# Kernel tuning notes

Hardware: AMD Instinct MI355X
Metric: run time of the kernel (lower is better)

The kernel has to match this reference:

```python
import jax, jax.numpy as jnp
import numpy as np

EPS = 1e-6
NUM_HEADS = 16
ROPE_THETA = 100000.0


def _rope_tables(seq_len, head_dim, theta):
    inv_freq = 1.0 / (theta ** (np.arange(0, head_dim, 2, dtype=np.float32) / head_dim))
    t = np.arange(seq_len, dtype=np.float32)
    freqs = np.outer(t, inv_freq)                      # (S, head_dim//2)
    emb = np.concatenate([freqs, freqs], axis=-1)      # (S, head_dim)
    return jnp.asarray(np.cos(emb))[None], jnp.asarray(np.sin(emb))[None]  # (1,S,D)


def setup_inputs() -> dict:
    key = jax.random.key(0)
    ks = jax.random.split(key, 6)
    B, S, H = 2, 2048, 1024
    head_dim = H // NUM_HEADS
    cos, sin = _rope_tables(S, head_dim, ROPE_THETA)
    scale = 0.02
    return {
        "hidden_states": jax.random.normal(ks[0], (B, S, H), dtype=jnp.float32),
        "cos": cos, "sin": sin,
        "Wq": jax.random.normal(ks[1], (H, H), dtype=jnp.float32) * scale,
        "bq": jnp.zeros((H,), dtype=jnp.float32),
        "Wk": jax.random.normal(ks[2], (H, H), dtype=jnp.float32) * scale,
        "bk": jnp.zeros((H,), dtype=jnp.float32),
        "Wv": jax.random.normal(ks[3], (H, H), dtype=jnp.float32) * scale,
        "bv": jnp.zeros((H,), dtype=jnp.float32),
        "Wo": jax.random.normal(ks[4], (H, H), dtype=jnp.float32) * scale,
        "bo": jnp.zeros((H,), dtype=jnp.float32),
        "rms_weight": jnp.ones((H,), dtype=jnp.float32),
    }


def _rms_norm(x, w):
    var = jnp.mean(x * x, axis=-1, keepdims=True)
    return x * jax.lax.rsqrt(var + EPS) * w


def _rotate_half(x):
    x1, x2 = jnp.split(x, 2, axis=-1)
    return jnp.concatenate([-x2, x1], axis=-1)


def reference(hidden_states, cos, sin, Wq, bq, Wk, bk, Wv, bv, Wo, bo, rms_weight):
    B, S, H = hidden_states.shape
    D = H // NUM_HEADS
    q = hidden_states @ Wq.T + bq
    k = hidden_states @ Wk.T + bk
    v = hidden_states @ Wv.T + bv
    # RMSNorm over full hidden dim BEFORE head split (as in original)
    q = _rms_norm(q, rms_weight)
    k = _rms_norm(k, rms_weight)
    # (B,S,H) -> (B,heads,S,D)
    q = q.reshape(B, S, NUM_HEADS, D).transpose(0, 2, 1, 3)
    k = k.reshape(B, S, NUM_HEADS, D).transpose(0, 2, 1, 3)
    v = v.reshape(B, S, NUM_HEADS, D).transpose(0, 2, 1, 3)
    # RoPE: cos/sin (1,S,D) -> unsqueeze head dim
    c = cos[:, None, :, :]
    s = sin[:, None, :, :]
    q = q * c + _rotate_half(q) * s
    k = k * c + _rotate_half(k) * s
    # attention (faithful: boolean tril mask is ADDED as 0/1, not -inf)
    scale = D ** 0.5
    scores = jnp.einsum("bhqd,bhkd->bhqk", q, k) / scale
    mask = jnp.tril(jnp.ones((S, S), dtype=scores.dtype))  # +1 on causal, +0 elsewhere
    attn = jax.nn.softmax(scores + mask, axis=-1)
    out = jnp.einsum("bhqk,bhkd->bhqd", attn, v)
    out = out.transpose(0, 2, 1, 3).reshape(B, S, H)
    return out @ Wo.T + bo
```

## Files before the change

kernel.cpp:

```cpp
#include <hip/hip_runtime.h>

typedef unsigned short u16;
typedef __attribute__((ext_vector_type(8))) _Float16 half8;
typedef __attribute__((ext_vector_type(2))) __fp16 fp16x2;
typedef __attribute__((ext_vector_type(4))) float f32x4;
typedef __attribute__((ext_vector_type(16))) float f32x16;

#define MFMAH(A,B,C) __builtin_amdgcn_mfma_f32_16x16x32_f16(A,B,C,0,0,0)
#define MFMA32(A,B,C) __builtin_amdgcn_mfma_f32_32x32x16_f16(A,B,C,0,0,0)
#define LOG2E 1.4426950408889634f
#define C1 0.18033688011112042f

__device__ __forceinline__ u16 f2h(float f){
  _Float16 h = (_Float16)f; u16 r; __builtin_memcpy(&r,&h,2); return r;
}
__device__ __forceinline__ float h2f(u16 v){
  _Float16 h; __builtin_memcpy(&h,&v,2); return (float)h;
}
__device__ __forceinline__ unsigned int pack_h2(float a, float b){
  fp16x2 h = __builtin_amdgcn_cvt_pkrtz(a,b);
  unsigned int r; __builtin_memcpy(&r,&h,4); return r;
}

__device__ __forceinline__ void async_ld16(const void* g, void* l) {
  __builtin_amdgcn_global_load_lds(
      (const __attribute__((address_space(1))) unsigned int*)g,
      (__attribute__((address_space(3))) unsigned int*)l, 16, 0, 0);
}

__global__ __launch_bounds__(256) void cast_all(const float* __restrict__ hs,
    const float* __restrict__ wq, const float* __restrict__ wk,
    const float* __restrict__ wv, const float* __restrict__ wo,
    u16* __restrict__ dst)
{
  unsigned int i = blockIdx.x*256 + threadIdx.x;
  size_t el = (size_t)i * 8;
  const float* src; size_t off;
  if (el < 4194304) { src = hs; off = el; }
  else {
    unsigned int r = (unsigned int)((el - 4194304) >> 20);
    src = (r==0)?wq:(r==1)?wk:(r==2)?wv:wo;
    off = (el - 4194304) & 1048575;
  }
  float4 a = *reinterpret_cast<const float4*>(src+off);
  float4 b = *reinterpret_cast<const float4*>(src+off+4);
  uint4 o = {pack_h2(a.x,a.y), pack_h2(a.z,a.w), pack_h2(b.x,b.y), pack_h2(b.z,b.w)};
  *reinterpret_cast<uint4*>(dst + el) = o;
}

__global__ __launch_bounds__(256) void gemm_qkv(const u16* __restrict__ A,
                                                const u16* __restrict__ W,
                                                const float* __restrict__ bqp,
                                                const float* __restrict__ bkp,
                                                const float* __restrict__ bvp,
                                                u16* __restrict__ qout,
                                                u16* __restrict__ kout,
                                                u16* __restrict__ vout,
                                                int M, int K)
{
  __shared__ __align__(16) u16 lds_a[128*32];
  __shared__ __align__(16) u16 lds_w[128*32];
  const int t = threadIdx.x;
  const int lane = t & 63, wave = t >> 6;
  const int wm = wave >> 1, wn = wave & 1;
  const int lr = lane & 15, quad = lane >> 4;
  const int flat = blockIdx.x;
  const int xcd = flat & 7, slot = flat >> 3;
  const int ln = slot % 12, lm = slot / 12;
  const int n0 = ((xcd & 1) * 12 + ln) * 128;
  const int m0 = ((xcd >> 1) * 8 + lm) * 128;
  const int wbase = t & 192;
  const int which = n0 >> 10;

  const f32x4 fzero = {0.f,0.f,0.f,0.f};
  f32x4 acc[4][4];
  #pragma unroll
  for (int i=0;i<4;++i)
    #pragma unroll
    for (int j=0;j<4;++j) acc[i][j] = fzero;

  if (which < 2) {
    for (int k0 = 0; k0 < K; k0 += 32) {
      __syncthreads();
      #pragma unroll
      for (int it=0; it<2; ++it) {
        int idx = it*256 + t;
        int row = idx >> 2, c8 = (idx & 3) * 8;
        int lbase = (it*256 + wbase) * 8;
        async_ld16(&A[(size_t)(m0+row)*K + k0 + c8], &lds_a[lbase]);
        async_ld16(&W[(size_t)(n0+row)*K + k0 + c8], &lds_w[lbase]);
      }
      __syncthreads();
      half8 af[4], bfr[4];
      #pragma unroll
      for (int mt=0; mt<4; ++mt)
        af[mt] = *reinterpret_cast<const half8*>(&lds_a[(wm*64 + mt*16 + lr)*32 + quad*8]);
      #pragma unroll
      for (int nt=0; nt<4; ++nt)
        bfr[nt] = *reinterpret_cast<const half8*>(&lds_w[(wn*64 + nt*16 + lr)*32 + quad*8]);
      #pragma unroll
      for (int mt=0; mt<4; ++mt)
        #pragma unroll
        for (int nt=0; nt<4; ++nt)
          acc[mt][nt] = MFMAH(bfr[nt], af[mt], acc[mt][nt]);
    }
    const float* bp = which ? bkp : bqp;
    u16* dst = which ? kout : qout;
    #pragma unroll
    for (int nt=0; nt<4; ++nt) {
      int nn = (n0 & 1023) + wn*64 + nt*16 + quad*4;
      float4 bv = *reinterpret_cast<const float4*>(&bp[nn]);
      int hh = nn >> 6, d4 = nn & 63;
      #pragma unroll
      for (int mt=0; mt<4; ++mt) {
        int m = m0 + wm*64 + mt*16 + lr;
        int b = m >> 11, s = m & 2047;
        uint2 o = {pack_h2(acc[mt][nt][0]+bv.x, acc[mt][nt][1]+bv.y),
                   pack_h2(acc[mt][nt][2]+bv.z, acc[mt][nt][3]+bv.w)};
        *reinterpret_cast<uint2*>(&dst[((size_t)(b*16 + hh)*2048 + s)*64 + d4]) = o;
      }
    }
  } else {
    for (int k0 = 0; k0 < K; k0 += 32) {
      __syncthreads();
      #pragma unroll
      for (int it=0; it<2; ++it) {
        int idx = it*256 + t;
        int row = idx >> 2, c8 = (idx & 3) * 8;
        int lbase = (it*256 + wbase) * 8;
        async_ld16(&A[(size_t)(m0+row)*K + k0 + c8], &lds_a[lbase]);
        async_ld16(&W[(size_t)(n0+row)*K + k0 + c8], &lds_w[lbase]);
      }
      __syncthreads();
      half8 af[4], bfr[4];
      #pragma unroll
      for (int mt=0; mt<4; ++mt)
        af[mt] = *reinterpret_cast<const half8*>(&lds_a[(wm*64 + mt*16 + lr)*32 + quad*8]);
      #pragma unroll
      for (int nt=0; nt<4; ++nt)
        bfr[nt] = *reinterpret_cast<const half8*>(&lds_w[(wn*64 + nt*16 + lr)*32 + quad*8]);
      #pragma unroll
      for (int mt=0; mt<4; ++mt)
        #pragma unroll
        for (int nt=0; nt<4; ++nt)
          acc[mt][nt] = MFMAH(af[mt], bfr[nt], acc[mt][nt]);
    }
    #pragma unroll
    for (int nt=0; nt<4; ++nt) {
      int nn = (n0 & 1023) + wn*64 + nt*16 + lr;
      float bv = bvp[nn];
      int hh = nn >> 6, d = nn & 63;
      #pragma unroll
      for (int mt=0; mt<4; ++mt) {
        int m = m0 + wm*64 + mt*16 + quad*4;
        int b = m >> 11, s = m & 2047;
        uint2 o = {pack_h2(acc[mt][nt][0]+bv, acc[mt][nt][1]+bv),
                   pack_h2(acc[mt][nt][2]+bv, acc[mt][nt][3]+bv)};
        *reinterpret_cast<uint2*>(&vout[((size_t)(b*16 + hh)*64 + d)*2048 + s]) = o;
      }
    }
  }
}

__global__ __launch_bounds__(256) void gemm_o(const u16* __restrict__ A,
                                              const u16* __restrict__ W,
                                              const float* __restrict__ bias,
                                              float* __restrict__ O,
                                              int M, int N, int K)
{
  __shared__ __align__(16) u16 lds_a[128*32];
  __shared__ __align__(16) u16 lds_w[64*32];
  const int t = threadIdx.x;
  const int lane = t & 63, wm = t >> 6;
  const int lr = lane & 15, quad = lane >> 4;
  const int flat = blockIdx.x;
  const int xcd = flat & 7, slot = flat >> 3;
  const int n0 = (slot & 15) * 64;
  const int m0 = ((xcd << 2) + (slot >> 4)) * 128;
  const int wbase = t & 192;

  const f32x4 fzero = {0.f,0.f,0.f,0.f};
  f32x4 acc[2][4];
  #pragma unroll
  for (int i=0;i<2;++i)
    #pragma unroll
    for (int j=0;j<4;++j) acc[i][j] = fzero;

  for (int k0 = 0; k0 < K; k0 += 32) {
    __syncthreads();
    #pragma unroll
    for (int it=0; it<2; ++it) {
      int idx = it*256 + t;
      int row = idx >> 2, c8 = (idx & 3) * 8;
      int lbase = (it*256 + wbase) * 8;
      async_ld16(&A[(size_t)(m0+row)*K + k0 + c8], &lds_a[lbase]);
    }
    async_ld16(&W[(size_t)(n0 + (t>>2))*K + k0 + (t&3)*8], &lds_w[wbase*8]);
    __syncthreads();
    half8 af[2], bfr[4];
    #pragma unroll
    for (int mt=0; mt<2; ++mt)
      af[mt] = *reinterpret_cast<const half8*>(&lds_a[(wm*32 + mt*16 + lr)*32 + quad*8]);
    #pragma unroll
    for (int nt=0; nt<4; ++nt)
      bfr[nt] = *reinterpret_cast<const half8*>(&lds_w[(nt*16 + lr)*32 + quad*8]);
    #pragma unroll
    for (int mt=0; mt<2; ++mt)
      #pragma unroll
      for (int nt=0; nt<4; ++nt)
        acc[mt][nt] = MFMAH(bfr[nt], af[mt], acc[mt][nt]);
  }

  #pragma unroll
  for (int nt=0; nt<4; ++nt) {
    int nb = n0 + nt*16 + quad*4;
    float4 bv = *reinterpret_cast<const float4*>(&bias[nb]);
    #pragma unroll
    for (int mt=0; mt<2; ++mt) {
      int m = m0 + wm*32 + mt*16 + lr;
      float4 o = {acc[mt][nt][0]+bv.x, acc[mt][nt][1]+bv.y,
                  acc[mt][nt][2]+bv.z, acc[mt][nt][3]+bv.w};
      *reinterpret_cast<float4*>(&O[(size_t)m * N + nb]) = o;
    }
  }
}

__global__ __launch_bounds__(256) void rmsrope(u16* __restrict__ qb, u16* __restrict__ kb,
                                               const float* __restrict__ cosb,
                                               const float* __restrict__ sinb,
                                               const float* __restrict__ w)
{
  const int bs = blockIdx.x;
  const int b = bs >> 11, s = bs & 2047;
  const int t = threadIdx.x;
  u16* buf = (t & 128) ? kb : qb;
  const int tl = t & 127;
  const int h = tl >> 3, d0 = (tl & 7) * 4;
  size_t base = ((size_t)(b*16+h)*2048 + s)*64;

  uint2 u1 = *reinterpret_cast<const uint2*>(&buf[base + d0]);
  uint2 u2 = *reinterpret_cast<const uint2*>(&buf[base + d0 + 32]);
  u16 a1[4], a2[4];
  __builtin_memcpy(a1, &u1, 8); __builtin_memcpy(a2, &u2, 8);
  float x1[4], x2[4];
  float ss = 0.f;
  #pragma unroll
  for (int j=0;j<4;++j){
    x1[j] = h2f(a1[j]); x2[j] = h2f(a2[j]);
    ss += x1[j]*x1[j] + x2[j]*x2[j];
  }
  #pragma unroll
  for (int off=32; off>0; off>>=1) ss += __shfl_xor(ss, off, 64);
  __shared__ float red[4];
  if ((t & 63) == 0) red[t>>6] = ss;
  __syncthreads();
  float tot = (t & 128) ? (red[2] + red[3]) : (red[0] + red[1]);
  float r = rsqrtf(tot * (1.0f/1024.0f) + 1e-6f);

  float4 w1 = *reinterpret_cast<const float4*>(&w[h*64+d0]);
  float4 w2 = *reinterpret_cast<const float4*>(&w[h*64+d0+32]);
  float4 c1 = *reinterpret_cast<const float4*>(&cosb[s*64+d0]);
  float4 s1 = *reinterpret_cast<const float4*>(&sinb[s*64+d0]);
  float4 c2 = *reinterpret_cast<const float4*>(&cosb[s*64+d0+32]);
  float4 s2 = *reinterpret_cast<const float4*>(&sinb[s*64+d0+32]);
  float n1[4] = {x1[0]*r*w1.x, x1[1]*r*w1.y, x1[2]*r*w1.z, x1[3]*r*w1.w};
  float n2[4] = {x2[0]*r*w2.x, x2[1]*r*w2.y, x2[2]*r*w2.z, x2[3]*r*w2.w};
  float o1[4] = {n1[0]*c1.x - n2[0]*s1.x, n1[1]*c1.y - n2[1]*s1.y,
                 n1[2]*c1.z - n2[2]*s1.z, n1[3]*c1.w - n2[3]*s1.w};
  float o2[4] = {n2[0]*c2.x + n1[0]*s2.x, n2[1]*c2.y + n1[1]*s2.y,
                 n2[2]*c2.z + n1[2]*s2.z, n2[3]*c2.w + n1[3]*s2.w};
  uint2 v1 = {pack_h2(o1[0],o1[1]), pack_h2(o1[2],o1[3])};
  uint2 v2 = {pack_h2(o2[0],o2[1]), pack_h2(o2[2],o2[3])};
  *reinterpret_cast<uint2*>(&buf[base + d0])      = v1;
  *reinterpret_cast<uint2*>(&buf[base + d0 + 32]) = v2;
}

__global__ __launch_bounds__(512, 2) void attn(const u16* __restrict__ qh,
                                               const u16* __restrict__ kh,
                                               const u16* __restrict__ vt,
                                               u16* __restrict__ ao)
{
  __shared__ __align__(16) u16 kbuf[2][2][64*72];
  __shared__ __align__(16) u16 vbuf[2][2][64*72];
  const int t = threadIdx.x;
  const int lane = t & 63, w = t >> 6;
  const int g = w >> 2, wq = w & 3;
  const int ql = lane & 31, hf = lane >> 5;
  const int flat = blockIdx.x;
  const int xcd = flat & 7, slot = flat >> 3;
  const int bh = xcd + ((slot >> 4) << 3);
  const int qbase = (slot & 15) * 128;
  const int b = bh >> 4, h = bh & 15;
  const size_t hb = (size_t)bh * 2048 * 64;
  const u16* qp = qh + hb;
  const u16* kp = kh + hb;
  const u16* vtp = vt + hb;

  const int q_abs = qbase + wq*32 + ql;
  half8 qf[4];
  #pragma unroll
  for (int s=0;s<4;++s)
    qf[s] = *reinterpret_cast<const half8*>(&qp[(size_t)q_abs*64 + s*16 + hf*8]);

  half8 onesf;
  #pragma unroll
  for (int i=0;i<8;++i) onesf[i] = (_Float16)1.0f;

  const int lt = t & 255;
  const int row = lt >> 3;
  const int cc = lt & 7;
  const int base2 = 32*(cc>>2) + 16*((cc>>1)&1) + 4*(cc&1);
  const int kofs = row*72 + cc*8;
  const u16* kg = kp + (size_t)(g*1024 + row)*64 + cc*8;
  const u16* vg = vtp + (size_t)row*2048 + g*1024 + base2;

  const f32x16 fz16 = {0.f,0.f,0.f,0.f,0.f,0.f,0.f,0.f,0.f,0.f,0.f,0.f,0.f,0.f,0.f,0.f};
  f32x16 oacc[2];
  oacc[0] = fz16; oacc[1] = fz16;
  f32x16 lacc = fz16;
  const int diag = (qbase + wq*32) >> 6;

  {
    uint4 k0v = *reinterpret_cast<const uint4*>(kg);
    uint4 k1v = *reinterpret_cast<const uint4*>(kg + 32*64);
    uint2 a0 = *reinterpret_cast<const uint2*>(vg);
    uint2 a1 = *reinterpret_cast<const uint2*>(vg + 8);
    uint2 b0 = *reinterpret_cast<const uint2*>(vg + (size_t)32*2048);
    uint2 b1 = *reinterpret_cast<const uint2*>(vg + (size_t)32*2048 + 8);
    *reinterpret_cast<uint4*>(&kbuf[g][0][kofs])        = k0v;
    *reinterpret_cast<uint4*>(&kbuf[g][0][kofs+32*72])  = k1v;
    uint4 v0 = {a0.x,a0.y,a1.x,a1.y};
    uint4 v1 = {b0.x,b0.y,b1.x,b1.y};
    *reinterpret_cast<uint4*>(&vbuf[g][0][kofs])        = v0;
    *reinterpret_cast<uint4*>(&vbuf[g][0][kofs+32*72])  = v1;
  }

  for (int kt=0; kt<16; ++kt) {
    __syncthreads();
    uint4 k0n, k1n; uint2 a0n, a1n, b0n, b1n;
    if (kt < 15) {
      const u16* kgn = kg + (size_t)(kt+1)*4096;
      const u16* vgn = vg + (kt+1)*64;
      k0n = *reinterpret_cast<const uint4*>(kgn);
      k1n = *reinterpret_cast<const uint4*>(kgn + 32*64);
      a0n = *reinterpret_cast<const uint2*>(vgn);
      a1n = *reinterpret_cast<const uint2*>(vgn + 8);
      b0n = *reinterpret_cast<const uint2*>(vgn + (size_t)32*2048);
      b1n = *reinterpret_cast<const uint2*>(vgn + (size_t)32*2048 + 8);
    }
    const u16* kb = &kbuf[g][kt & 1][0];
    const u16* vb = &vbuf[g][kt & 1][0];
    const int gkt = (g << 4) + kt;

    unsigned int pk[4][4];
    #pragma unroll
    for (int kh2=0; kh2<2; ++kh2) {
      f32x16 z = fz16;
      #pragma unroll
      for (int s=0;s<4;++s) {
        half8 kf;
        __builtin_memcpy(&kf, &kb[(kh2*32+ql)*72 + s*16 + hf*8], 16);
        z = MFMA32(kf, qf[s], z);
      }
      float p[16];
      if (gkt != diag) {
        float ml = (gkt < diag) ? LOG2E : 0.0f;
        #pragma unroll
        for (int r=0;r<16;++r)
          p[r] = __builtin_amdgcn_exp2f(__builtin_fmaf(z[r], C1, ml));
      } else {
        #pragma unroll
        for (int r=0;r<16;++r) {
          int key = gkt*64 + kh2*32 + (r&3) + 8*(r>>2) + 4*hf;
          float ml = (key <= q_abs) ? LOG2E : 0.0f;
          p[r] = __builtin_amdgcn_exp2f(__builtin_fmaf(z[r], C1, ml));
        }
      }
      #pragma unroll
      for (int t2=0;t2<2;++t2)
        #pragma unroll
        for (int jj=0;jj<4;++jj)
          pk[kh2*2+t2][jj] = pack_h2(p[t2*8+jj*2], p[t2*8+jj*2+1]);
    }

    #pragma unroll
    for (int st=0;st<4;++st) {
      uint4 pq = {pk[st][0], pk[st][1], pk[st][2], pk[st][3]};
      half8 pf; __builtin_memcpy(&pf, &pq, 16);
      lacc = MFMA32(onesf, pf, lacc);
      #pragma unroll
      for (int dh=0; dh<2; ++dh) {
        half8 vf;
        __builtin_memcpy(&vf, &vb[(dh*32+ql)*72 + st*16 + hf*8], 16);
        oacc[dh] = MFMA32(vf, pf, oacc[dh]);
      }
    }

    if (kt < 15) {
      u16* kwn = &kbuf[g][(kt+1)&1][kofs];
      u16* vwn = &vbuf[g][(kt+1)&1][kofs];
      *reinterpret_cast<uint4*>(kwn)         = k0n;
      *reinterpret_cast<uint4*>(kwn + 32*72) = k1n;
      uint4 v0 = {a0n.x,a0n.y,a1n.x,a1n.y};
      uint4 v1 = {b0n.x,b0n.y,b1n.x,b1n.y};
      *reinterpret_cast<uint4*>(vwn)         = v0;
      *reinterpret_cast<uint4*>(vwn + 32*72) = v1;
    }
  }

  __syncthreads();
  f32x4* xch4 = (f32x4*)&kbuf[0][0][0];
  float* xls  = (float*)&vbuf[0][0][0];
  const int idx = wq*64 + lane;
  if (g == 1) {
    #pragma unroll
    for (int dh=0; dh<2; ++dh)
      #pragma unroll
      for (int rq=0; rq<4; ++rq) {
        f32x4 v = {oacc[dh][rq*4+0], oacc[dh][rq*4+1],
                   oacc[dh][rq*4+2], oacc[dh][rq*4+3]};
        xch4[(dh*4+rq)*256 + idx] = v;
      }
    xls[idx] = lacc[0];
  }
  __syncthreads();
  if (g == 0) {
    float inv = 1.0f / (lacc[0] + xls[idx]);
    size_t rowbase = ((size_t)(b*2048 + q_abs))*1024 + h*64;
    #pragma unroll
    for (int dh=0; dh<2; ++dh)
      #pragma unroll
      for (int rq=0; rq<4; ++rq) {
        int dd = dh*32 + 8*rq + 4*hf;
        f32x4 v = xch4[(dh*4+rq)*256 + idx];
        uint2 o = {pack_h2((oacc[dh][rq*4+0]+v.x)*inv, (oacc[dh][rq*4+1]+v.y)*inv),
                   pack_h2((oacc[dh][rq*4+2]+v.z)*inv, (oacc[dh][rq*4+3]+v.w)*inv)};
        *reinterpret_cast<uint2*>(&ao[rowbase + dd]) = o;
      }
  }
}

extern "C" void kernel_launch(void* const* d_in, const int* in_sizes, int n_in,
                              void* d_out, int out_size, void* d_ws, size_t ws_size,
                              hipStream_t stream)
{
  const float* hs   = (const float*)d_in[0];
  const float* cosb = (const float*)d_in[1];
  const float* sinb = (const float*)d_in[2];
  const float* Wq   = (const float*)d_in[3];
  const float* bq   = (const float*)d_in[4];
  const float* Wk   = (const float*)d_in[5];
  const float* bk   = (const float*)d_in[6];
  const float* Wv   = (const float*)d_in[7];
  const float* bv   = (const float*)d_in[8];
  const float* Wo   = (const float*)d_in[9];
  const float* bo   = (const float*)d_in[10];
  const float* rw   = (const float*)d_in[11];

  const size_t NEL = (size_t)4096 * 1024;
  const size_t WEL = (size_t)1024 * 1024;
  u16* hsb = (u16*)d_ws;
  u16* wqb = hsb + NEL;
  u16* wob = wqb + 3*WEL;
  u16* qhb = wob + WEL;
  u16* khb = qhb + NEL;
  u16* vtb = khb + NEL;
  u16* aob = hsb;

  cast_all<<<4096, 256, 0, stream>>>(hs, Wq, Wk, Wv, Wo, hsb);
  gemm_qkv<<<768, 256, 0, stream>>>(hsb, wqb, bq, bk, bv, qhb, khb, vtb, 4096, 1024);
  rmsrope<<<4096, 256, 0, stream>>>(qhb, khb, cosb, sinb, rw);
  attn<<<512, 512, 0, stream>>>(qhb, khb, vtb, aob);
  gemm_o<<<512, 256, 0, stream>>>(aob, wob, bo, (float*)d_out, 4096, 1024, 1024);
}
```

Measured before the change: 219.4 us.

## Process two 32-row query tiles per wave in attention to reuse K/V fragments

Each wave now handles 64 query rows (two 32-row tiles) instead of 32, so every K and V fragment loaded from LDS feeds two MFMAs. The grid halves to 256 blocks and launch bounds drop to one block per CU to make room for the doubled accumulators. The row-sum MFMA against a ones vector is replaced by scalar accumulation of the probabilities plus a cross-half shuffle. The aim is less LDS traffic and fewer MFMAs per output. The cost is higher register pressure, lower occupancy and only 256 blocks, which may underfill the GPU's compute units.

```diff
diff --git a/kernel.cpp b/kernel.cpp
--- a/kernel.cpp
+++ b/kernel.cpp
@@ -275,7 +275,7 @@
   *reinterpret_cast<uint2*>(&buf[base + d0 + 32]) = v2;
 }
 
-__global__ __launch_bounds__(512, 2) void attn(const u16* __restrict__ qh,
+__global__ __launch_bounds__(512, 1) void attn(const u16* __restrict__ qh,
                                                const u16* __restrict__ kh,
                                                const u16* __restrict__ vt,
                                                u16* __restrict__ ao)
@@ -288,23 +288,22 @@
   const int ql = lane & 31, hf = lane >> 5;
   const int flat = blockIdx.x;
   const int xcd = flat & 7, slot = flat >> 3;
-  const int bh = xcd + ((slot >> 4) << 3);
-  const int qbase = (slot & 15) * 128;
+  const int bh = xcd + ((slot >> 3) << 3);
+  const int qbase = (slot & 7) * 256;
   const int b = bh >> 4, h = bh & 15;
   const size_t hb = (size_t)bh * 2048 * 64;
   const u16* qp = qh + hb;
   const u16* kp = kh + hb;
   const u16* vtp = vt + hb;
 
-  const int q_abs = qbase + wq*32 + ql;
-  half8 qf[4];
+  half8 qf[2][4];
   #pragma unroll
-  for (int s=0;s<4;++s)
-    qf[s] = *reinterpret_cast<const half8*>(&qp[(size_t)q_abs*64 + s*16 + hf*8]);
-
-  half8 onesf;
-  #pragma unroll
-  for (int i=0;i<8;++i) onesf[i] = (_Float16)1.0f;
+  for (int qh2=0; qh2<2; ++qh2) {
+    int qa = qbase + wq*64 + qh2*32 + ql;
+    #pragma unroll
+    for (int s=0;s<4;++s)
+      qf[qh2][s] = *reinterpret_cast<const half8*>(&qp[(size_t)qa*64 + s*16 + hf*8]);
+  }
 
   const int lt = t & 255;
   const int row = lt >> 3;
@@ -315,10 +314,10 @@
   const u16* vg = vtp + (size_t)row*2048 + g*1024 + base2;
 
   const f32x16 fz16 = {0.f,0.f,0.f,0.f,0.f,0.f,0.f,0.f,0.f,0.f,0.f,0.f,0.f,0.f,0.f,0.f};
-  f32x16 oacc[2];
-  oacc[0] = fz16; oacc[1] = fz16;
-  f32x16 lacc = fz16;
-  const int diag = (qbase + wq*32) >> 6;
+  f32x16 oacc[2][2];
+  oacc[0][0]=fz16; oacc[0][1]=fz16; oacc[1][0]=fz16; oacc[1][1]=fz16;
+  float lsum[2] = {0.f, 0.f};
+  const int diag = (qbase + wq*64) >> 6;
 
   {
     uint4 k0v = *reinterpret_cast<const uint4*>(kg);
@@ -352,47 +351,60 @@
     const u16* vb = &vbuf[g][kt & 1][0];
     const int gkt = (g << 4) + kt;
 
-    unsigned int pk[4][4];
+    unsigned int pk[2][4][4];
     #pragma unroll
     for (int kh2=0; kh2<2; ++kh2) {
-      f32x16 z = fz16;
-      #pragma unroll
-      for (int s=0;s<4;++s) {
-        half8 kf;
-        __builtin_memcpy(&kf, &kb[(kh2*32+ql)*72 + s*16 + hf*8], 16);
-        z = MFMA32(kf, qf[s], z);
+      half8 kf[4];
+      #pragma unroll
+      for (int s=0;s<4;++s)
+        __builtin_memcpy(&kf[s], &kb[(kh2*32+ql)*72 + s*16 + hf*8], 16);
+      f32x16 z0 = fz16, z1 = fz16;
+      #pragma unroll
+      for (int s=0;s<4;++s) z0 = MFMA32(kf[s], qf[0][s], z0);
+      #pragma unroll
+      for (int s=0;s<4;++s) z1 = MFMA32(kf[s], qf[1][s], z1);
+
+      #pragma unroll
+      for (int qh2=0; qh2<2; ++qh2) {
+        const f32x16& z = qh2 ? z1 : z0;
+        const int qa = qbase + wq*64 + qh2*32 + ql;
+        float p[16];
+        if (gkt != diag) {
+          float ml = (gkt < diag) ? LOG2E : 0.0f;
+          #pragma unroll
+          for (int r=0;r<16;++r)
+            p[r] = __builtin_amdgcn_exp2f(__builtin_fmaf(z[r], C1, ml));
+        } else {
+          #pragma unroll
+          for (int r=0;r<16;++r) {
+            int key = gkt*64 + kh2*32 + (r&3) + 8*(r>>2) + 4*hf;
+            float ml = (key <= qa) ? LOG2E : 0.0f;
+            p[r] = __builtin_amdgcn_exp2f(__builtin_fmaf(z[r], C1, ml));
+          }
+        }
+        float ls0=0.f, ls1=0.f, ls2=0.f, ls3=0.f;
+        #pragma unroll
+        for (int r=0;r<16;r+=4){ ls0+=p[r]; ls1+=p[r+1]; ls2+=p[r+2]; ls3+=p[r+3]; }
+        lsum[qh2] += (ls0+ls1)+(ls2+ls3);
+        #pragma unroll
+        for (int t2=0;t2<2;++t2)
+          #pragma unroll
+          for (int jj=0;jj<4;++jj)
+            pk[qh2][kh2*2+t2][jj] = pack_h2(p[t2*8+jj*2], p[t2*8+jj*2+1]);
       }
-      float p[16];
-      if (gkt != diag) {
-        float ml = (gkt < diag) ? LOG2E : 0.0f;
-        #pragma unroll
-        for (int r=0;r<16;++r)
-          p[r] = __builtin_amdgcn_exp2f(__builtin_fmaf(z[r], C1, ml));
-      } else {
-        #pragma unroll
-        for (int r=0;r<16;++r) {
-          int key = gkt*64 + kh2*32 + (r&3) + 8*(r>>2) + 4*hf;
-          float ml = (key <= q_abs) ? LOG2E : 0.0f;
-          p[r] = __builtin_amdgcn_exp2f(__builtin_fmaf(z[r], C1, ml));
-        }
-      }
-      #pragma unroll
-      for (int t2=0;t2<2;++t2)
-        #pragma unroll
-        for (int jj=0;jj<4;++jj)
-          pk[kh2*2+t2][jj] = pack_h2(p[t2*8+jj*2], p[t2*8+jj*2+1]);
     }
 
     #pragma unroll
     for (int st=0;st<4;++st) {
-      uint4 pq = {pk[st][0], pk[st][1], pk[st][2], pk[st][3]};
-      half8 pf; __builtin_memcpy(&pf, &pq, 16);
-      lacc = MFMA32(onesf, pf, lacc);
-      #pragma unroll
-      for (int dh=0; dh<2; ++dh) {
-        half8 vf;
-        __builtin_memcpy(&vf, &vb[(dh*32+ql)*72 + st*16 + hf*8], 16);
-        oacc[dh] = MFMA32(vf, pf, oacc[dh]);
+      half8 vf0, vf1;
+      __builtin_memcpy(&vf0, &vb[(0*32+ql)*72 + st*16 + hf*8], 16);
+      __builtin_memcpy(&vf1, &vb[(1*32+ql)*72 + st*16 + hf*8], 16);
+      #pragma unroll
+      for (int qh2=0; qh2<2; ++qh2) {
+        uint4 pq = {pk[qh2][st][0], pk[qh2][st][1], pk[qh2][st][2], pk[qh2][st][3]};
+        half8 pf; __builtin_memcpy(&pf, &pq, 16);
+        oacc[qh2][0] = MFMA32(vf0, pf, oacc[qh2][0]);
+        oacc[qh2][1] = MFMA32(vf1, pf, oacc[qh2][1]);
       }
     }
 
@@ -408,35 +420,48 @@
     }
   }
 
+  lsum[0] += __shfl_xor(lsum[0], 32, 64);
+  lsum[1] += __shfl_xor(lsum[1], 32, 64);
+
   __syncthreads();
-  f32x4* xch4 = (f32x4*)&kbuf[0][0][0];
-  float* xls  = (float*)&vbuf[0][0][0];
+  f32x4* xch0 = (f32x4*)&kbuf[0][0][0];
+  f32x4* xch1 = (f32x4*)&vbuf[0][0][0];
+  float* xls  = (float*)((char*)&vbuf[0][0][0] + 32768);
   const int idx = wq*64 + lane;
   if (g == 1) {
     #pragma unroll
-    for (int dh=0; dh<2; ++dh)
-      #pragma unroll
-      for (int rq=0; rq<4; ++rq) {
-        f32x4 v = {oacc[dh][rq*4+0], oacc[dh][rq*4+1],
-                   oacc[dh][rq*4+2], oacc[dh][rq*4+3]};
-        xch4[(dh*4+rq)*256 + idx] = v;
-      }
-    xls[idx] = lacc[0];
+    for (int qh2=0; qh2<2; ++qh2) {
+      f32x4* xch = qh2 ? xch1 : xch0;
+      #pragma unroll
+      for (int dh=0; dh<2; ++dh)
+        #pragma unroll
+        for (int rq=0; rq<4; ++rq) {
+          f32x4 v = {oacc[qh2][dh][rq*4+0], oacc[qh2][dh][rq*4+1],
+                     oacc[qh2][dh][rq*4+2], oacc[qh2][dh][rq*4+3]};
+          xch[(dh*4+rq)*256 + idx] = v;
+        }
+      xls[qh2*256 + idx] = lsum[qh2];
+    }
   }
   __syncthreads();
   if (g == 0) {
-    float inv = 1.0f / (lacc[0] + xls[idx]);
-    size_t rowbase = ((size_t)(b*2048 + q_abs))*1024 + h*64;
-    #pragma unroll
-    for (int dh=0; dh<2; ++dh)
-      #pragma unroll
-      for (int rq=0; rq<4; ++rq) {
-        int dd = dh*32 + 8*rq + 4*hf;
-        f32x4 v = xch4[(dh*4+rq)*256 + idx];
-        uint2 o = {pack_h2((oacc[dh][rq*4+0]+v.x)*inv, (oacc[dh][rq*4+1]+v.y)*inv),
-                   pack_h2((oacc[dh][rq*4+2]+v.z)*inv, (oacc[dh][rq*4+3]+v.w)*inv)};
-        *reinterpret_cast<uint2*>(&ao[rowbase + dd]) = o;
-      }
+    #pragma unroll
+    for (int qh2=0; qh2<2; ++qh2) {
+      f32x4* xch = qh2 ? xch1 : xch0;
+      float inv = 1.0f / (lsum[qh2] + xls[qh2*256 + idx]);
+      int qa = qbase + wq*64 + qh2*32 + ql;
+      size_t rowbase = ((size_t)(b*2048 + qa))*1024 + h*64;
+      #pragma unroll
+      for (int dh=0; dh<2; ++dh)
+        #pragma unroll
+        for (int rq=0; rq<4; ++rq) {
+          int dd = dh*32 + 8*rq + 4*hf;
+          f32x4 v = xch[(dh*4+rq)*256 + idx];
+          uint2 o = {pack_h2((oacc[qh2][dh][rq*4+0]+v.x)*inv, (oacc[qh2][dh][rq*4+1]+v.y)*inv),
+                     pack_h2((oacc[qh2][dh][rq*4+2]+v.z)*inv, (oacc[qh2][dh][rq*4+3]+v.w)*inv)};
+          *reinterpret_cast<uint2*>(&ao[rowbase + dd]) = o;
+        }
+    }
   }
 }
 
@@ -470,6 +495,6 @@
   cast_all<<<4096, 256, 0, stream>>>(hs, Wq, Wk, Wv, Wo, hsb);
   gemm_qkv<<<768, 256, 0, stream>>>(hsb, wqb, bq, bk, bv, qhb, khb, vtb, 4096, 1024);
   rmsrope<<<4096, 256, 0, stream>>>(qhb, khb, cosb, sinb, rw);
-  attn<<<512, 512, 0, stream>>>(qhb, khb, vtb, aob);
+  attn<<<256, 512, 0, stream>>>(qhb, khb, vtb, aob);
   gemm_o<<<512, 256, 0, stream>>>(aob, wob, bo, (float*)d_out, 4096, 1024, 1024);
 }
```

After: 213.3 us (median of 19 runs). -2.8%, faster.
